# Optimization experiments

Hardware: AMD Instinct MI355X
Metric: run time of the kernel (lower is better)

The kernel has to match this reference:

```python
import jax, jax.numpy as jnp
import numpy as np
from jax.ops import segment_sum

N_NODES = 500_000
N_EDGES = 16_000_000


def gcn_conv(x, W, b, src, dst, n_nodes):
    """PyG GCNConv: linear transform, add self-loops, sym deg norm, scatter-add."""
    xw = x @ W  # [N, out]
    # degree including self-loop (edge weight 1 each)
    deg = segment_sum(jnp.ones((src.shape[0],), xw.dtype), dst, num_segments=n_nodes) + 1.0
    dinv = jax.lax.rsqrt(deg)  # deg^{-1/2}, deg >= 1 so safe
    norm = dinv[src] * dinv[dst]  # [E]
    msg = xw[src] * norm[:, None]  # [E, out]
    agg = segment_sum(msg, dst, num_segments=n_nodes)
    # self-loop contribution: norm_ii = dinv_i^2
    agg = agg + xw * (dinv * dinv)[:, None]
    return agg + b


def setup_inputs() -> dict:
    key = jax.random.key(0)
    ks = jax.random.split(key, 8)
    x = jax.random.normal(ks[0], (N_NODES, 2), dtype=jnp.float32)
    edge_index = jax.random.randint(ks[1], (2, N_EDGES), 0, N_NODES, dtype=jnp.int64)
    def glorot(k, fan_in, fan_out):
        s = jnp.sqrt(6.0 / (fan_in + fan_out))
        return jax.random.uniform(k, (fan_in, fan_out), jnp.float32, -s, s)
    return {
        "x": x,
        "edge_index": edge_index,
        "W1": glorot(ks[2], 2, 4), "b1": jnp.zeros((4,), jnp.float32),
        "W2": glorot(ks[3], 4, 4), "b2": jnp.zeros((4,), jnp.float32),
        "W3": glorot(ks[4], 4, 2), "b3": jnp.zeros((2,), jnp.float32),
    }


def reference(x, edge_index, W1, b1, W2, b2, W3, b3):
    src, dst = edge_index[0], edge_index[1]
    n = x.shape[0]
    h = jnp.tanh(gcn_conv(x, W1, b1, src, dst, n))
    h = jnp.tanh(gcn_conv(h, W2, b2, src, dst, n))
    h = gcn_conv(h, W3, b3, src, dst, n)
    return h
```

## Files before the change

### kernel.cpp

```cpp
#include <hip/hip_runtime.h>
#include <hip/hip_fp16.h>


#define TPB 256
#define T_TILE 16384
#define SBB 12
#define NSB_MAX 128
#define FINE_BITS 10
#define EB_CAP 34048


__global__ void __launch_bounds__(512)
count1(const int* __restrict__ dst, int* __restrict__ cnt1, int ntB, int E, int SB) {
    __shared__ int hist[NSB_MAX];
    int blk = blockIdx.x, tid = threadIdx.x;
    if (tid < SB) hist[tid] = 0;
    __syncthreads();
    int base = blk * T_TILE;
    #pragma unroll 8
    for (int it = 0; it < T_TILE / 512; ++it) {
        int e = base + it * 512 + tid;
        if (e < E) atomicAdd(&hist[((unsigned)dst[e]) >> SBB], 1);
    }
    __syncthreads();
    if (tid < SB) cnt1[(size_t)tid * ntB + blk] = hist[tid];
}

__global__ void scan_k1(const int* __restrict__ data, int* __restrict__ bsum, int len) {
    __shared__ int lds[TPB];
    int b = blockIdx.x, t = threadIdx.x;
    int base = b * 1024 + t * 4;
    int s = 0;
    #pragma unroll
    for (int j = 0; j < 4; ++j) { int i = base + j; if (i < len) s += data[i]; }
    lds[t] = s; __syncthreads();
    for (int off = 128; off > 0; off >>= 1) {
        if (t < off) lds[t] += lds[t + off];
        __syncthreads();
    }
    if (t == 0) bsum[b] = lds[0];
}

__global__ void scan_k2(int* __restrict__ bsum, int NB) {
    __shared__ int lds[1024];
    int t = threadIdx.x;
    int v = (t < NB) ? bsum[t] : 0;
    lds[t] = v; __syncthreads();
    for (int off = 1; off < 1024; off <<= 1) {
        int add = (t >= off) ? lds[t - off] : 0;
        __syncthreads();
        lds[t] += add;
        __syncthreads();
    }
    if (t < NB) bsum[t] = lds[t] - v;
}

__global__ void scan_k3(int* __restrict__ data, const int* __restrict__ bsum, int len) {
    __shared__ int lds[TPB];
    int b = blockIdx.x, t = threadIdx.x;
    int base = b * 1024 + t * 4;
    int v[4]; int s = 0;
    #pragma unroll
    for (int j = 0; j < 4; ++j) { int i = base + j; v[j] = (i < len) ? data[i] : 0; s += v[j]; }
    int orig = s;
    lds[t] = s; __syncthreads();
    for (int off = 1; off < 256; off <<= 1) {
        int add = (t >= off) ? lds[t - off] : 0;
        __syncthreads();
        lds[t] += add;
        __syncthreads();
    }
    int run = bsum[b] + lds[t] - orig;
    #pragma unroll
    for (int j = 0; j < 4; ++j) {
        int i = base + j;
        if (i < len) { data[i] = run; run += v[j]; }
    }
}

__global__ void bases_fix(const int* __restrict__ cnt1, int ntB, int SB,
                          int* __restrict__ bases1, int* __restrict__ rowptr,
                          int N, int E) {
    int t = threadIdx.x;
    if (t < SB) bases1[t] = cnt1[(size_t)t * ntB];
    if (t == 0) { bases1[SB] = E; rowptr[N] = E; }
}

__global__ void __launch_bounds__(512)
scatter1(const int* __restrict__ dst, const int* __restrict__ src,
         const int* __restrict__ cnt1, unsigned* __restrict__ pk1,
         int ntB, int E, int SB) {
    __shared__ unsigned lpk[T_TILE];
    __shared__ int lhist[NSB_MAX];
    __shared__ int lexcl[NSB_MAX];
    __shared__ int lcur[NSB_MAX];
    __shared__ int basec[NSB_MAX];
    int blk = blockIdx.x, tid = threadIdx.x;
    if (tid < NSB_MAX) lhist[tid] = 0;
    if (tid < SB) basec[tid] = cnt1[(size_t)tid * ntB + blk];
    __syncthreads();
    int base = blk * T_TILE;
    #pragma unroll 8
    for (int it = 0; it < T_TILE / 512; ++it) {
        int e = base + it * 512 + tid;
        if (e < E) atomicAdd(&lhist[((unsigned)dst[e]) >> SBB], 1);
    }
    __syncthreads();
    int hv = (tid < NSB_MAX) ? lhist[tid] : 0;
    if (tid < NSB_MAX) lexcl[tid] = hv;
    __syncthreads();
    for (int off = 1; off < NSB_MAX; off <<= 1) {
        int a = (tid < NSB_MAX && tid >= off) ? lexcl[tid - off] : 0;
        __syncthreads();
        if (tid < NSB_MAX) lexcl[tid] += a;
        __syncthreads();
    }
    if (tid < NSB_MAX) { lexcl[tid] -= hv; lcur[tid] = lexcl[tid]; }
    __syncthreads();
    #pragma unroll 8
    for (int it = 0; it < T_TILE / 512; ++it) {
        int e = base + it * 512 + tid;
        if (e < E) {
            unsigned d = (unsigned)dst[e];
            unsigned s = (unsigned)src[e];
            int pos = atomicAdd(&lcur[d >> SBB], 1);
            lpk[pos] = (d & 4095u) | (s << SBB);
        }
    }
    __syncthreads();
    for (int b = 0; b < SB; ++b) {
        int lo = lexcl[b], cntb = lhist[b], gb = basec[b];
        for (int t2 = tid; t2 < cntb; t2 += 512)
            pk1[gb + t2] = lpk[lo + t2];
    }
}

__global__ void __launch_bounds__(1024)
buildfine(const int* __restrict__ bases1, const unsigned* __restrict__ pk1,
          const float* __restrict__ x, int* __restrict__ rowptr,
          float* __restrict__ dinv, unsigned* __restrict__ z1h,
          unsigned* __restrict__ csr, int N) {
    __shared__ int cnt[1024];
    __shared__ int tmp[1024];
    __shared__ int cur[1024];
    __shared__ unsigned eb[EB_CAP];
    __shared__ int redbase;
    int bid = blockIdx.x, tid = threadIdx.x;
    int sb = bid >> 2, j = bid & 3;
    int node0 = (sb << SBB) + (j << FINE_BITS);
    int ebeg = bases1[sb], eend = bases1[sb + 1];
    int n = eend - ebeg;
    cnt[tid] = 0;
    if (tid == 0) redbase = 0;
    __syncthreads();
    int lane = tid & 63;
    int myprev = 0;
    int k0 = 0;
    for (; k0 + 8192 <= n; k0 += 8192) {
        unsigned p[8];
        #pragma unroll
        for (int u = 0; u < 8; ++u) p[u] = pk1[ebeg + k0 + tid + u * 1024];
        #pragma unroll
        for (int u = 0; u < 8; ++u) {
            int f = (int)((p[u] >> FINE_BITS) & 3u);
            myprev += (int)__popcll(__ballot(f < j));
            if (f == j) atomicAdd(&cnt[p[u] & 1023u], 1);
        }
    }
    for (int kk = k0; kk < n; kk += 1024) {
        int k = kk + tid;
        bool valid = (k < n);
        unsigned p = valid ? pk1[ebeg + k] : 0u;
        int f = valid ? (int)((p >> FINE_BITS) & 3u) : 4;
        myprev += (int)__popcll(__ballot(valid && f < j));
        if (valid && f == j) atomicAdd(&cnt[p & 1023u], 1);
    }
    if (lane == 0 && myprev > 0) atomicAdd(&redbase, myprev);
    __syncthreads();
    int csr_base = ebeg + redbase;
    int c = cnt[tid];
    tmp[tid] = c; __syncthreads();
    for (int o = 1; o < 1024; o <<= 1) {
        int a = (tid >= o) ? tmp[tid - o] : 0;
        __syncthreads();
        tmp[tid] += a;
        __syncthreads();
    }
    int excl = tmp[tid] - c;
    int tot = tmp[1023];
    int i = node0 + tid;
    if (i < N) {
        rowptr[i] = csr_base + excl;
        float di = rsqrtf((float)c + 1.0f);
        dinv[i] = di;
        float2 xv = ((const float2*)x)[i];
        __half2 hz = __floats2half2_rn(xv.x * di, xv.y * di);
        z1h[i] = *(unsigned*)&hz;
    }
    cur[tid] = excl;
    __syncthreads();
    if (tot <= EB_CAP) {
        k0 = 0;
        for (; k0 + 8192 <= n; k0 += 8192) {
            unsigned p[8];
            #pragma unroll
            for (int u = 0; u < 8; ++u) p[u] = pk1[ebeg + k0 + tid + u * 1024];
            #pragma unroll
            for (int u = 0; u < 8; ++u) {
                if (((p[u] >> FINE_BITS) & 3u) == (unsigned)j) {
                    int pos = atomicAdd(&cur[p[u] & 1023u], 1);
                    eb[pos] = p[u] >> SBB;
                }
            }
        }
        for (int k = k0 + tid; k < n; k += 1024) {
            unsigned p = pk1[ebeg + k];
            if (((p >> FINE_BITS) & 3u) == (unsigned)j) {
                int pos = atomicAdd(&cur[p & 1023u], 1);
                eb[pos] = p >> SBB;
            }
        }
        __syncthreads();
        for (int k = tid; k < tot; k += 1024) csr[csr_base + k] = eb[k];
    } else {
        for (int k = tid; k < n; k += 1024) {
            unsigned p = pk1[ebeg + k];
            if (((p >> FINE_BITS) & 3u) == (unsigned)j) {
                int pos = atomicAdd(&cur[p & 1023u], 1);
                csr[csr_base + pos] = p >> SBB;
            }
        }
    }
}


__global__ void gcn1(const int* __restrict__ rowptr, const unsigned* __restrict__ csr,
                     const unsigned* __restrict__ z1h, const float* __restrict__ W1,
                     const float* __restrict__ b1, const float* __restrict__ dinv,
                     uint2* __restrict__ z2h, int N) {
    int i = blockIdx.x * blockDim.x + threadIdx.x;
    if (i >= N) return;
    int r0 = rowptr[i], r1 = rowptr[i + 1];
    float a0, a1;
    {
        unsigned zr = z1h[i];
        float2 zi = __half22float2(*(__half2*)&zr);
        a0 = zi.x; a1 = zi.y;
    }
    int k = r0;
    for (; k + 16 <= r1; k += 16) {
        unsigned j[16];
        #pragma unroll
        for (int u = 0; u < 16; ++u) j[u] = __builtin_nontemporal_load(&csr[k + u]);
        unsigned raw[16];
        #pragma unroll
        for (int u = 0; u < 16; ++u) raw[u] = z1h[j[u]];
        #pragma unroll
        for (int u = 0; u < 16; ++u) {
            float2 v = __half22float2(*(__half2*)&raw[u]);
            a0 += v.x; a1 += v.y;
        }
    }
    for (; k < r1; ++k) {
        unsigned zr = z1h[csr[k]];
        float2 zv = __half22float2(*(__half2*)&zr);
        a0 += zv.x; a1 += zv.y;
    }
    float di = dinv[i];
    float g0 = di * a0, g1 = di * a1;
    float o0 = di * tanhf(fmaf(g0, W1[0], fmaf(g1, W1[4], b1[0])));
    float o1 = di * tanhf(fmaf(g0, W1[1], fmaf(g1, W1[5], b1[1])));
    float o2 = di * tanhf(fmaf(g0, W1[2], fmaf(g1, W1[6], b1[2])));
    float o3 = di * tanhf(fmaf(g0, W1[3], fmaf(g1, W1[7], b1[3])));
    __half2 ha = __floats2half2_rn(o0, o1);
    __half2 hb = __floats2half2_rn(o2, o3);
    uint2 packed;
    packed.x = *(unsigned*)&ha;
    packed.y = *(unsigned*)&hb;
    z2h[i] = packed;
}

__global__ void gcn2(const int* __restrict__ rowptr, const unsigned* __restrict__ csr,
                     const uint2* __restrict__ z2h, const float* __restrict__ W2,
                     const float* __restrict__ b2, const float* __restrict__ W3,
                     const float* __restrict__ dinv, unsigned* __restrict__ z3h, int N) {
    int i = blockIdx.x * blockDim.x + threadIdx.x;
    if (i >= N) return;
    int r0 = rowptr[i], r1 = rowptr[i + 1];
    float a0, a1, a2, a3;
    {
        uint2 raw = z2h[i];
        float2 f01 = __half22float2(*(__half2*)&raw.x);
        float2 f23 = __half22float2(*(__half2*)&raw.y);
        a0 = f01.x; a1 = f01.y; a2 = f23.x; a3 = f23.y;
    }
    int k = r0;
    for (; k + 8 <= r1; k += 8) {
        unsigned j[8];
        #pragma unroll
        for (int u = 0; u < 8; ++u) j[u] = __builtin_nontemporal_load(&csr[k + u]);
        uint2 raw[8];
        #pragma unroll
        for (int u = 0; u < 8; ++u) raw[u] = z2h[j[u]];
        #pragma unroll
        for (int u = 0; u < 8; ++u) {
            float2 f01 = __half22float2(*(__half2*)&raw[u].x);
            float2 f23 = __half22float2(*(__half2*)&raw[u].y);
            a0 += f01.x; a1 += f01.y; a2 += f23.x; a3 += f23.y;
        }
    }
    for (; k < r1; ++k) {
        uint2 raw = z2h[csr[k]];
        float2 f01 = __half22float2(*(__half2*)&raw.x);
        float2 f23 = __half22float2(*(__half2*)&raw.y);
        a0 += f01.x; a1 += f01.y; a2 += f23.x; a3 += f23.y;
    }
    float di = dinv[i];
    float g0 = di * a0, g1 = di * a1, g2 = di * a2, g3 = di * a3;
    float h[4];
    #pragma unroll
    for (int c = 0; c < 4; ++c)
        h[c] = tanhf(b2[c] + g0 * W2[c] + g1 * W2[4 + c] + g2 * W2[8 + c] + g3 * W2[12 + c]);
    float v0 = h[0] * W3[0] + h[1] * W3[2] + h[2] * W3[4] + h[3] * W3[6];
    float v1 = h[0] * W3[1] + h[1] * W3[3] + h[2] * W3[5] + h[3] * W3[7];
    __half2 hz = __floats2half2_rn(v0 * di, v1 * di);
    z3h[i] = *(unsigned*)&hz;
}

__global__ void gcn3(const int* __restrict__ rowptr, const unsigned* __restrict__ csr,
                     const unsigned* __restrict__ z3h, const float* __restrict__ b3,
                     const float* __restrict__ dinv, float* __restrict__ out, int N) {
    int i = blockIdx.x * blockDim.x + threadIdx.x;
    if (i >= N) return;
    int r0 = rowptr[i], r1 = rowptr[i + 1];
    float a0, a1;
    {
        unsigned zr = z3h[i];
        float2 zi = __half22float2(*(__half2*)&zr);
        a0 = zi.x; a1 = zi.y;
    }
    int k = r0;
    for (; k + 16 <= r1; k += 16) {
        unsigned j[16];
        #pragma unroll
        for (int u = 0; u < 16; ++u) j[u] = __builtin_nontemporal_load(&csr[k + u]);
        unsigned raw[16];
        #pragma unroll
        for (int u = 0; u < 16; ++u) raw[u] = z3h[j[u]];
        #pragma unroll
        for (int u = 0; u < 16; ++u) {
            float2 v = __half22float2(*(__half2*)&raw[u]);
            a0 += v.x; a1 += v.y;
        }
    }
    for (; k < r1; ++k) {
        unsigned zr = z3h[csr[k]];
        float2 zv = __half22float2(*(__half2*)&zr);
        a0 += zv.x; a1 += zv.y;
    }
    float di = dinv[i];
    ((float2*)out)[i] = make_float2(fmaf(di, a0, b3[0]), fmaf(di, a1, b3[1]));
}

extern "C" void kernel_launch(void* const* d_in, const int* in_sizes, int n_in,
                              void* d_out, int out_size, void* d_ws, size_t ws_size,
                              hipStream_t stream) {
    const float* x  = (const float*)d_in[0];
    const int*   ei = (const int*)d_in[1];
    const float* W1 = (const float*)d_in[2];
    const float* b1 = (const float*)d_in[3];
    const float* W2 = (const float*)d_in[4];
    const float* b2 = (const float*)d_in[5];
    const float* W3 = (const float*)d_in[6];
    const float* b3 = (const float*)d_in[7];
    float* out = (float*)d_out;

    const int N = in_sizes[0] / 2;
    const int E = in_sizes[1] / 2;
    const int* src = ei;
    const int* dst = ei + E;

    const int SB  = (N + (1 << SBB) - 1) >> SBB;
    const int ntB = (E + T_TILE - 1) / T_TILE;
    const int mlen = SB * ntB;
    const int NB = (mlen + 1023) / 1024;

    auto align = [](size_t o) { return (o + 255) & ~(size_t)255; };
    char* wbase = (char*)d_ws;
    size_t off = 0;
    float*    dinv   = (float*)(wbase + off);    off = align(off + (size_t)N * 4);
    unsigned* z1h    = (unsigned*)(wbase + off); off = align(off + (size_t)N * 4);
    uint2*    z2h    = (uint2*)(wbase + off);    off = align(off + (size_t)N * 8);
    unsigned* z3h    = (unsigned*)(wbase + off); off = align(off + (size_t)N * 4);
    int*      rowptr = (int*)(wbase + off);      off = align(off + (size_t)(N + 1) * 4);
    int*      bsum   = (int*)(wbase + off);      off = align(off + (size_t)1024 * 4);
    int*      bases1 = (int*)(wbase + off);      off = align(off + (size_t)(SB + 1) * 4);
    int*      cnt1   = (int*)(wbase + off);      off = align(off + (size_t)mlen * 4);
    unsigned* pk1    = (unsigned*)(wbase + off); off = align(off + (size_t)E * 4);
    unsigned* csr    = (unsigned*)(wbase + off); off = align(off + (size_t)E * 4);

    dim3 gN((N + TPB - 1) / TPB);
    count1<<<dim3(ntB), dim3(512), 0, stream>>>(dst, cnt1, ntB, E, SB);
    scan_k1<<<dim3(NB), dim3(TPB), 0, stream>>>(cnt1, bsum, mlen);
    scan_k2<<<dim3(1), dim3(1024), 0, stream>>>(bsum, NB);
    scan_k3<<<dim3(NB), dim3(TPB), 0, stream>>>(cnt1, bsum, mlen);
    bases_fix<<<dim3(1), dim3(256), 0, stream>>>(cnt1, ntB, SB, bases1, rowptr, N, E);
    scatter1<<<dim3(ntB), dim3(512), 0, stream>>>(dst, src, cnt1, pk1, ntB, E, SB);
    buildfine<<<dim3(SB * 4), dim3(1024), 0, stream>>>(bases1, pk1, x, rowptr, dinv,
                                                       z1h, csr, N);
    gcn1<<<gN, dim3(TPB), 0, stream>>>(rowptr, csr, z1h, W1, b1, dinv, z2h, N);
    gcn2<<<gN, dim3(TPB), 0, stream>>>(rowptr, csr, z2h, W2, b2, W3, dinv, z3h, N);
    gcn3<<<gN, dim3(TPB), 0, stream>>>(rowptr, csr, z3h, b3, dinv, out, N);
}
```

Before: 781.2 us.

## Split layer-2 gather into two passes by source-node half for cache locality

Each CSR row is partitioned so that edges whose source lies in the lower half of the node range come first, and a split pointer is recorded per row. Layer 2 then becomes two kernels: the first gathers only from the lower half of z2h and writes fp32 partial sums, and the second gathers from the upper half, adds the partials and applies the dense transform. Keeping each pass's gather working set to half the feature table (about 2 MB) is meant to improve L2 hit rates on random gathers. The cost is an extra kernel launch, a 16 B-per-node partial-sum round trip, a second row-pointer array, and extra LDS atomics in buildfine.

```diff
diff --git a/kernel.cpp b/kernel.cpp
--- a/kernel.cpp
+++ b/kernel.cpp
@@ -138,11 +138,14 @@
 __global__ void __launch_bounds__(1024)
 buildfine(const int* __restrict__ bases1, const unsigned* __restrict__ pk1,
           const float* __restrict__ x, int* __restrict__ rowptr,
-          float* __restrict__ dinv, unsigned* __restrict__ z1h,
-          unsigned* __restrict__ csr, int N) {
-    __shared__ int cnt[1024];
+          int* __restrict__ splitr, float* __restrict__ dinv,
+          unsigned* __restrict__ z1h, unsigned* __restrict__ csr,
+          int N, unsigned NHP) {
+    __shared__ int cntT[1024];
+    __shared__ int cntA[1024];
     __shared__ int tmp[1024];
-    __shared__ int cur[1024];
+    __shared__ int curA[1024];
+    __shared__ int curB[1024];
     __shared__ unsigned eb[EB_CAP];
     __shared__ int redbase;
     int bid = blockIdx.x, tid = threadIdx.x;
@@ -150,7 +153,7 @@
     int node0 = (sb << SBB) + (j << FINE_BITS);
     int ebeg = bases1[sb], eend = bases1[sb + 1];
     int n = eend - ebeg;
-    cnt[tid] = 0;
+    cntT[tid] = 0; cntA[tid] = 0;
     if (tid == 0) redbase = 0;
     __syncthreads();
     int lane = tid & 63;
@@ -164,7 +167,11 @@
         for (int u = 0; u < 8; ++u) {
             int f = (int)((p[u] >> FINE_BITS) & 3u);
             myprev += (int)__popcll(__ballot(f < j));
-            if (f == j) atomicAdd(&cnt[p[u] & 1023u], 1);
+            if (f == j) {
+                unsigned nd = p[u] & 1023u;
+                atomicAdd(&cntT[nd], 1);
+                if (p[u] < NHP) atomicAdd(&cntA[nd], 1);
+            }
         }
     }
     for (int kk = k0; kk < n; kk += 1024) {
@@ -173,12 +180,17 @@
         unsigned p = valid ? pk1[ebeg + k] : 0u;
         int f = valid ? (int)((p >> FINE_BITS) & 3u) : 4;
         myprev += (int)__popcll(__ballot(valid && f < j));
-        if (valid && f == j) atomicAdd(&cnt[p & 1023u], 1);
+        if (valid && f == j) {
+            unsigned nd = p & 1023u;
+            atomicAdd(&cntT[nd], 1);
+            if (p < NHP) atomicAdd(&cntA[nd], 1);
+        }
     }
     if (lane == 0 && myprev > 0) atomicAdd(&redbase, myprev);
     __syncthreads();
     int csr_base = ebeg + redbase;
-    int c = cnt[tid];
+    int c = cntT[tid];
+    int ca = cntA[tid];
     tmp[tid] = c; __syncthreads();
     for (int o = 1; o < 1024; o <<= 1) {
         int a = (tid >= o) ? tmp[tid - o] : 0;
@@ -191,13 +203,15 @@
     int i = node0 + tid;
     if (i < N) {
         rowptr[i] = csr_base + excl;
+        splitr[i] = csr_base + excl + ca;
         float di = rsqrtf((float)c + 1.0f);
         dinv[i] = di;
         float2 xv = ((const float2*)x)[i];
         __half2 hz = __floats2half2_rn(xv.x * di, xv.y * di);
         z1h[i] = *(unsigned*)&hz;
     }
-    cur[tid] = excl;
+    curA[tid] = excl;
+    curB[tid] = excl + ca;
     __syncthreads();
     if (tot <= EB_CAP) {
         k0 = 0;
@@ -208,7 +222,9 @@
             #pragma unroll
             for (int u = 0; u < 8; ++u) {
                 if (((p[u] >> FINE_BITS) & 3u) == (unsigned)j) {
-                    int pos = atomicAdd(&cur[p[u] & 1023u], 1);
+                    unsigned nd = p[u] & 1023u;
+                    int* cp = (p[u] < NHP) ? curA : curB;
+                    int pos = atomicAdd(&cp[nd], 1);
                     eb[pos] = p[u] >> SBB;
                 }
             }
@@ -216,7 +232,9 @@
         for (int k = k0 + tid; k < n; k += 1024) {
             unsigned p = pk1[ebeg + k];
             if (((p >> FINE_BITS) & 3u) == (unsigned)j) {
-                int pos = atomicAdd(&cur[p & 1023u], 1);
+                unsigned nd = p & 1023u;
+                int* cp = (p < NHP) ? curA : curB;
+                int pos = atomicAdd(&cp[nd], 1);
                 eb[pos] = p >> SBB;
             }
         }
@@ -226,7 +244,9 @@
         for (int k = tid; k < n; k += 1024) {
             unsigned p = pk1[ebeg + k];
             if (((p >> FINE_BITS) & 3u) == (unsigned)j) {
-                int pos = atomicAdd(&cur[p & 1023u], 1);
+                unsigned nd = p & 1023u;
+                int* cp = (p < NHP) ? curA : curB;
+                int pos = atomicAdd(&cp[nd], 1);
                 csr[csr_base + pos] = p >> SBB;
             }
         }
@@ -280,21 +300,73 @@
     z2h[i] = packed;
 }
 
-__global__ void gcn2(const int* __restrict__ rowptr, const unsigned* __restrict__ csr,
-                     const uint2* __restrict__ z2h, const float* __restrict__ W2,
-                     const float* __restrict__ b2, const float* __restrict__ W3,
-                     const float* __restrict__ dinv, unsigned* __restrict__ z3h, int N) {
+__global__ void gcn2a(const int* __restrict__ rowptr, const int* __restrict__ splitr,
+                      const unsigned* __restrict__ csr, const uint2* __restrict__ z2h,
+                      unsigned long long* __restrict__ part, int N, unsigned NH) {
     int i = blockIdx.x * blockDim.x + threadIdx.x;
     if (i >= N) return;
-    int r0 = rowptr[i], r1 = rowptr[i + 1];
-    float a0, a1, a2, a3;
-    {
+    int r0 = rowptr[i], rs = splitr[i];
+    float a0 = 0.f, a1 = 0.f, a2 = 0.f, a3 = 0.f;
+    if ((unsigned)i < NH) {
         uint2 raw = z2h[i];
         float2 f01 = __half22float2(*(__half2*)&raw.x);
         float2 f23 = __half22float2(*(__half2*)&raw.y);
         a0 = f01.x; a1 = f01.y; a2 = f23.x; a3 = f23.y;
     }
     int k = r0;
+    for (; k + 8 <= rs; k += 8) {
+        unsigned j[8];
+        #pragma unroll
+        for (int u = 0; u < 8; ++u) j[u] = __builtin_nontemporal_load(&csr[k + u]);
+        uint2 raw[8];
+        #pragma unroll
+        for (int u = 0; u < 8; ++u) raw[u] = z2h[j[u]];
+        #pragma unroll
+        for (int u = 0; u < 8; ++u) {
+            float2 f01 = __half22float2(*(__half2*)&raw[u].x);
+            float2 f23 = __half22float2(*(__half2*)&raw[u].y);
+            a0 += f01.x; a1 += f01.y; a2 += f23.x; a3 += f23.y;
+        }
+    }
+    for (; k < rs; ++k) {
+        uint2 raw = z2h[csr[k]];
+        float2 f01 = __half22float2(*(__half2*)&raw.x);
+        float2 f23 = __half22float2(*(__half2*)&raw.y);
+        a0 += f01.x; a1 += f01.y; a2 += f23.x; a3 += f23.y;
+    }
+    unsigned long long p0 = (unsigned long long)__float_as_uint(a0) |
+                            ((unsigned long long)__float_as_uint(a1) << 32);
+    unsigned long long p1 = (unsigned long long)__float_as_uint(a2) |
+                            ((unsigned long long)__float_as_uint(a3) << 32);
+    __builtin_nontemporal_store(p0, &part[2 * (size_t)i]);
+    __builtin_nontemporal_store(p1, &part[2 * (size_t)i + 1]);
+}
+
+__global__ void gcn2b(const int* __restrict__ rowptr, const int* __restrict__ splitr,
+                      const unsigned* __restrict__ csr, const uint2* __restrict__ z2h,
+                      const float* __restrict__ W2, const float* __restrict__ b2,
+                      const float* __restrict__ W3, const float* __restrict__ dinv,
+                      const unsigned long long* __restrict__ part,
+                      unsigned* __restrict__ z3h, int N, unsigned NH) {
+    int i = blockIdx.x * blockDim.x + threadIdx.x;
+    if (i >= N) return;
+    int rs = splitr[i], r1 = rowptr[i + 1];
+    float a0, a1, a2, a3;
+    {
+        unsigned long long p0 = __builtin_nontemporal_load(&part[2 * (size_t)i]);
+        unsigned long long p1 = __builtin_nontemporal_load(&part[2 * (size_t)i + 1]);
+        a0 = __uint_as_float((unsigned)p0);
+        a1 = __uint_as_float((unsigned)(p0 >> 32));
+        a2 = __uint_as_float((unsigned)p1);
+        a3 = __uint_as_float((unsigned)(p1 >> 32));
+    }
+    if ((unsigned)i >= NH) {
+        uint2 raw = z2h[i];
+        float2 f01 = __half22float2(*(__half2*)&raw.x);
+        float2 f23 = __half22float2(*(__half2*)&raw.y);
+        a0 += f01.x; a1 += f01.y; a2 += f23.x; a3 += f23.y;
+    }
+    int k = rs;
     for (; k + 8 <= r1; k += 8) {
         unsigned j[8];
         #pragma unroll
@@ -384,6 +456,8 @@
     const int ntB = (E + T_TILE - 1) / T_TILE;
     const int mlen = SB * ntB;
     const int NB = (mlen + 1023) / 1024;
+    const unsigned NH  = (unsigned)(N / 2);
+    const unsigned NHP = NH << SBB;
 
     auto align = [](size_t o) { return (o + 255) & ~(size_t)255; };
     char* wbase = (char*)d_ws;
@@ -392,7 +466,10 @@
     unsigned* z1h    = (unsigned*)(wbase + off); off = align(off + (size_t)N * 4);
     uint2*    z2h    = (uint2*)(wbase + off);    off = align(off + (size_t)N * 8);
     unsigned* z3h    = (unsigned*)(wbase + off); off = align(off + (size_t)N * 4);
+    unsigned long long* part = (unsigned long long*)(wbase + off);
+    off = align(off + (size_t)N * 16);
     int*      rowptr = (int*)(wbase + off);      off = align(off + (size_t)(N + 1) * 4);
+    int*      splitr = (int*)(wbase + off);      off = align(off + (size_t)N * 4);
     int*      bsum   = (int*)(wbase + off);      off = align(off + (size_t)1024 * 4);
     int*      bases1 = (int*)(wbase + off);      off = align(off + (size_t)(SB + 1) * 4);
     int*      cnt1   = (int*)(wbase + off);      off = align(off + (size_t)mlen * 4);
@@ -406,9 +483,11 @@
     scan_k3<<<dim3(NB), dim3(TPB), 0, stream>>>(cnt1, bsum, mlen);
     bases_fix<<<dim3(1), dim3(256), 0, stream>>>(cnt1, ntB, SB, bases1, rowptr, N, E);
     scatter1<<<dim3(ntB), dim3(512), 0, stream>>>(dst, src, cnt1, pk1, ntB, E, SB);
-    buildfine<<<dim3(SB * 4), dim3(1024), 0, stream>>>(bases1, pk1, x, rowptr, dinv,
-                                                       z1h, csr, N);
+    buildfine<<<dim3(SB * 4), dim3(1024), 0, stream>>>(bases1, pk1, x, rowptr, splitr,
+                                                       dinv, z1h, csr, N, NHP);
     gcn1<<<gN, dim3(TPB), 0, stream>>>(rowptr, csr, z1h, W1, b1, dinv, z2h, N);
-    gcn2<<<gN, dim3(TPB), 0, stream>>>(rowptr, csr, z2h, W2, b2, W3, dinv, z3h, N);
+    gcn2a<<<gN, dim3(TPB), 0, stream>>>(rowptr, splitr, csr, z2h, part, N, NH);
+    gcn2b<<<gN, dim3(TPB), 0, stream>>>(rowptr, splitr, csr, z2h, W2, b2, W3, dinv,
+                                        part, z3h, N, NH);
     gcn3<<<gN, dim3(TPB), 0, stream>>>(rowptr, csr, z3h, b3, dinv, out, N);
 }
```

After: 787.5 us. No clear change (+0.8%).

## Replace per-node CSR pull with LDS-accumulated push over source-bucketed edges

Applied to the files above, without the earlier changes.

Drops the full per-node CSR build (fine 4-way split, prefix scans, LDS staging) and instead buckets each destination region's edges by source super-block. Each layer then runs a push kernel where a block gathers source features and accumulates into a 4096-node LDS accumulator with shared-memory float atomics, writing per-quarter partials that a finalize kernel reduces and activates. This aims to make the source gathers more cache-local and to remove the divergent per-row loops, at the cost of LDS atomic contention, partial-buffer traffic and nondeterministic float summation order.

```diff
diff --git a/kernel.cpp b/kernel.cpp
--- a/kernel.cpp
+++ b/kernel.cpp
@@ -6,8 +6,6 @@
 #define T_TILE 16384
 #define SBB 12
 #define NSB_MAX 128
-#define FINE_BITS 10
-#define EB_CAP 34048
 
 
 __global__ void __launch_bounds__(512)
@@ -79,11 +77,10 @@
 }
 
 __global__ void bases_fix(const int* __restrict__ cnt1, int ntB, int SB,
-                          int* __restrict__ bases1, int* __restrict__ rowptr,
-                          int N, int E) {
+                          int* __restrict__ bases1, int E) {
     int t = threadIdx.x;
     if (t < SB) bases1[t] = cnt1[(size_t)t * ntB];
-    if (t == 0) { bases1[SB] = E; rowptr[N] = E; }
+    if (t == 0) bases1[SB] = E;
 }
 
 __global__ void __launch_bounds__(512)
@@ -136,135 +133,172 @@
 }
 
 __global__ void __launch_bounds__(1024)
-buildfine(const int* __restrict__ bases1, const unsigned* __restrict__ pk1,
-          const float* __restrict__ x, int* __restrict__ rowptr,
-          float* __restrict__ dinv, unsigned* __restrict__ z1h,
-          unsigned* __restrict__ csr, int N) {
-    __shared__ int cnt[1024];
-    __shared__ int tmp[1024];
-    __shared__ int cur[1024];
-    __shared__ unsigned eb[EB_CAP];
-    __shared__ int redbase;
-    int bid = blockIdx.x, tid = threadIdx.x;
-    int sb = bid >> 2, j = bid & 3;
-    int node0 = (sb << SBB) + (j << FINE_BITS);
-    int ebeg = bases1[sb], eend = bases1[sb + 1];
+buildpush(const int* __restrict__ bases1, const unsigned* __restrict__ pk1,
+          const float* __restrict__ x, float* __restrict__ dinv,
+          unsigned* __restrict__ z1h, unsigned* __restrict__ pk2,
+          int* __restrict__ tb, int N) {
+    __shared__ int deg[4096];
+    __shared__ int hist[16][NSB_MAX];
+    __shared__ int cnt[NSB_MAX];
+    __shared__ int cur[NSB_MAX];
+    int reg = blockIdx.x, tid = threadIdx.x;
+    int ebeg = bases1[reg], eend = bases1[reg + 1];
     int n = eend - ebeg;
-    cnt[tid] = 0;
-    if (tid == 0) redbase = 0;
-    __syncthreads();
-    int lane = tid & 63;
-    int myprev = 0;
-    int k0 = 0;
-    for (; k0 + 8192 <= n; k0 += 8192) {
-        unsigned p[8];
-        #pragma unroll
-        for (int u = 0; u < 8; ++u) p[u] = pk1[ebeg + k0 + tid + u * 1024];
-        #pragma unroll
-        for (int u = 0; u < 8; ++u) {
-            int f = (int)((p[u] >> FINE_BITS) & 3u);
-            myprev += (int)__popcll(__ballot(f < j));
-            if (f == j) atomicAdd(&cnt[p[u] & 1023u], 1);
+    int w = tid >> 6;
+    for (int i = tid; i < 4096; i += 1024) deg[i] = 0;
+    for (int i = tid; i < 16 * NSB_MAX; i += 1024) ((int*)hist)[i] = 0;
+    __syncthreads();
+    for (int k = tid; k < n; k += 1024) {
+        unsigned p = pk1[ebeg + k];
+        atomicAdd(&deg[p & 4095u], 1);
+        atomicAdd(&hist[w][p >> 24], 1);
+    }
+    __syncthreads();
+    if (tid < NSB_MAX) {
+        int s = 0;
+        #pragma unroll
+        for (int r = 0; r < 16; ++r) s += hist[r][tid];
+        cnt[tid] = s;
+        cur[tid] = s;
+    }
+    __syncthreads();
+    for (int off = 1; off < NSB_MAX; off <<= 1) {
+        int a = (tid < NSB_MAX && tid >= off) ? cur[tid - off] : 0;
+        __syncthreads();
+        if (tid < NSB_MAX) cur[tid] += a;
+        __syncthreads();
+    }
+    if (tid < NSB_MAX) {
+        int excl = cur[tid] - cnt[tid];
+        tb[reg * 129 + tid] = ebeg + excl;
+        cur[tid] = excl;
+    }
+    if (tid == 0) tb[reg * 129 + 128] = eend;
+    int node0 = reg << SBB;
+    for (int t = tid; t < 4096; t += 1024) {
+        int i = node0 + t;
+        if (i < N) {
+            float di = rsqrtf((float)deg[t] + 1.0f);
+            dinv[i] = di;
+            float2 xv = ((const float2*)x)[i];
+            __half2 hz = __floats2half2_rn(xv.x * di, xv.y * di);
+            z1h[i] = *(unsigned*)&hz;
         }
     }
-    for (int kk = k0; kk < n; kk += 1024) {
-        int k = kk + tid;
-        bool valid = (k < n);
-        unsigned p = valid ? pk1[ebeg + k] : 0u;
-        int f = valid ? (int)((p >> FINE_BITS) & 3u) : 4;
-        myprev += (int)__popcll(__ballot(valid && f < j));
-        if (valid && f == j) atomicAdd(&cnt[p & 1023u], 1);
-    }
-    if (lane == 0 && myprev > 0) atomicAdd(&redbase, myprev);
-    __syncthreads();
-    int csr_base = ebeg + redbase;
-    int c = cnt[tid];
-    tmp[tid] = c; __syncthreads();
-    for (int o = 1; o < 1024; o <<= 1) {
-        int a = (tid >= o) ? tmp[tid - o] : 0;
-        __syncthreads();
-        tmp[tid] += a;
-        __syncthreads();
-    }
-    int excl = tmp[tid] - c;
-    int tot = tmp[1023];
-    int i = node0 + tid;
-    if (i < N) {
-        rowptr[i] = csr_base + excl;
-        float di = rsqrtf((float)c + 1.0f);
-        dinv[i] = di;
-        float2 xv = ((const float2*)x)[i];
-        __half2 hz = __floats2half2_rn(xv.x * di, xv.y * di);
-        z1h[i] = *(unsigned*)&hz;
-    }
-    cur[tid] = excl;
-    __syncthreads();
-    if (tot <= EB_CAP) {
-        k0 = 0;
-        for (; k0 + 8192 <= n; k0 += 8192) {
-            unsigned p[8];
-            #pragma unroll
-            for (int u = 0; u < 8; ++u) p[u] = pk1[ebeg + k0 + tid + u * 1024];
-            #pragma unroll
-            for (int u = 0; u < 8; ++u) {
-                if (((p[u] >> FINE_BITS) & 3u) == (unsigned)j) {
-                    int pos = atomicAdd(&cur[p[u] & 1023u], 1);
-                    eb[pos] = p[u] >> SBB;
-                }
-            }
+    __syncthreads();
+    for (int k = tid; k < n; k += 1024) {
+        unsigned p = pk1[ebeg + k];
+        int pos = atomicAdd(&cur[p >> 24], 1);
+        pk2[ebeg + pos] = p;
+    }
+}
+
+
+__global__ void __launch_bounds__(512)
+push_f2(const unsigned* __restrict__ pk2, const int* __restrict__ tb,
+        const unsigned* __restrict__ zt, float* __restrict__ partial) {
+    __shared__ float acc[8192];
+    int bx = blockIdx.x, tid = threadIdx.x;
+    int reg = bx >> 2, s = bx & 3;
+    for (int i = tid; i < 8192; i += 512) acc[i] = 0.f;
+    __syncthreads();
+    int e0 = tb[reg * 129 + 32 * s];
+    int e1 = tb[reg * 129 + 32 * (s + 1)];
+    int k = e0;
+    for (; k + 2048 <= e1; k += 2048) {
+        unsigned p[4];
+        #pragma unroll
+        for (int u = 0; u < 4; ++u) p[u] = __builtin_nontemporal_load(&pk2[k + tid + u * 512]);
+        unsigned zr[4];
+        #pragma unroll
+        for (int u = 0; u < 4; ++u) zr[u] = zt[p[u] >> SBB];
+        #pragma unroll
+        for (int u = 0; u < 4; ++u) {
+            float2 v = __half22float2(*(__half2*)&zr[u]);
+            unsigned d = (p[u] & 4095u) << 1;
+            atomicAdd(&acc[d], v.x);
+            atomicAdd(&acc[d + 1], v.y);
         }
-        for (int k = k0 + tid; k < n; k += 1024) {
-            unsigned p = pk1[ebeg + k];
-            if (((p >> FINE_BITS) & 3u) == (unsigned)j) {
-                int pos = atomicAdd(&cur[p & 1023u], 1);
-                eb[pos] = p >> SBB;
-            }
+    }
+    for (int kk = k + tid; kk < e1; kk += 512) {
+        unsigned p = pk2[kk];
+        unsigned zr = zt[p >> SBB];
+        float2 v = __half22float2(*(__half2*)&zr);
+        unsigned d = (p & 4095u) << 1;
+        atomicAdd(&acc[d], v.x);
+        atomicAdd(&acc[d + 1], v.y);
+    }
+    __syncthreads();
+    float* pout = partial + (size_t)bx * 8192;
+    for (int i = tid; i < 8192; i += 512) pout[i] = acc[i];
+}
+
+__global__ void __launch_bounds__(512)
+push_f4(const unsigned* __restrict__ pk2, const int* __restrict__ tb,
+        const unsigned long long* __restrict__ zt, float* __restrict__ partial) {
+    __shared__ float acc[16384];
+    int bx = blockIdx.x, tid = threadIdx.x;
+    int reg = bx >> 2, s = bx & 3;
+    for (int i = tid; i < 16384; i += 512) acc[i] = 0.f;
+    __syncthreads();
+    int e0 = tb[reg * 129 + 32 * s];
+    int e1 = tb[reg * 129 + 32 * (s + 1)];
+    int k = e0;
+    for (; k + 2048 <= e1; k += 2048) {
+        unsigned p[4];
+        #pragma unroll
+        for (int u = 0; u < 4; ++u) p[u] = __builtin_nontemporal_load(&pk2[k + tid + u * 512]);
+        unsigned long long zr[4];
+        #pragma unroll
+        for (int u = 0; u < 4; ++u) zr[u] = zt[p[u] >> SBB];
+        #pragma unroll
+        for (int u = 0; u < 4; ++u) {
+            unsigned lo = (unsigned)zr[u], hi = (unsigned)(zr[u] >> 32);
+            float2 f01 = __half22float2(*(__half2*)&lo);
+            float2 f23 = __half22float2(*(__half2*)&hi);
+            unsigned d = (p[u] & 4095u) << 2;
+            atomicAdd(&acc[d], f01.x);
+            atomicAdd(&acc[d + 1], f01.y);
+            atomicAdd(&acc[d + 2], f23.x);
+            atomicAdd(&acc[d + 3], f23.y);
         }
-        __syncthreads();
-        for (int k = tid; k < tot; k += 1024) csr[csr_base + k] = eb[k];
-    } else {
-        for (int k = tid; k < n; k += 1024) {
-            unsigned p = pk1[ebeg + k];
-            if (((p >> FINE_BITS) & 3u) == (unsigned)j) {
-                int pos = atomicAdd(&cur[p & 1023u], 1);
-                csr[csr_base + pos] = p >> SBB;
-            }
-        }
-    }
-}
-
-
-__global__ void gcn1(const int* __restrict__ rowptr, const unsigned* __restrict__ csr,
-                     const unsigned* __restrict__ z1h, const float* __restrict__ W1,
-                     const float* __restrict__ b1, const float* __restrict__ dinv,
-                     uint2* __restrict__ z2h, int N) {
+    }
+    for (int kk = k + tid; kk < e1; kk += 512) {
+        unsigned p = pk2[kk];
+        unsigned long long zr = zt[p >> SBB];
+        unsigned lo = (unsigned)zr, hi = (unsigned)(zr >> 32);
+        float2 f01 = __half22float2(*(__half2*)&lo);
+        float2 f23 = __half22float2(*(__half2*)&hi);
+        unsigned d = (p & 4095u) << 2;
+        atomicAdd(&acc[d], f01.x);
+        atomicAdd(&acc[d + 1], f01.y);
+        atomicAdd(&acc[d + 2], f23.x);
+        atomicAdd(&acc[d + 3], f23.y);
+    }
+    __syncthreads();
+    float* pout = partial + (size_t)bx * 16384;
+    for (int i = tid; i < 16384; i += 512) pout[i] = acc[i];
+}
+
+
+__global__ void fin1(const float* __restrict__ partial, const unsigned* __restrict__ z1h,
+                     const float* __restrict__ dinv, const float* __restrict__ W1,
+                     const float* __restrict__ b1, unsigned long long* __restrict__ z2h,
+                     int N) {
     int i = blockIdx.x * blockDim.x + threadIdx.x;
     if (i >= N) return;
-    int r0 = rowptr[i], r1 = rowptr[i + 1];
+    int reg = i >> SBB, t = i & 4095;
     float a0, a1;
     {
         unsigned zr = z1h[i];
-        float2 zi = __half22float2(*(__half2*)&zr);
-        a0 = zi.x; a1 = zi.y;
-    }
-    int k = r0;
-    for (; k + 16 <= r1; k += 16) {
-        unsigned j[16];
-        #pragma unroll
-        for (int u = 0; u < 16; ++u) j[u] = __builtin_nontemporal_load(&csr[k + u]);
-        unsigned raw[16];
-        #pragma unroll
-        for (int u = 0; u < 16; ++u) raw[u] = z1h[j[u]];
-        #pragma unroll
-        for (int u = 0; u < 16; ++u) {
-            float2 v = __half22float2(*(__half2*)&raw[u]);
-            a0 += v.x; a1 += v.y;
-        }
-    }
-    for (; k < r1; ++k) {
-        unsigned zr = z1h[csr[k]];
-        float2 zv = __half22float2(*(__half2*)&zr);
-        a0 += zv.x; a1 += zv.y;
+        float2 z = __half22float2(*(__half2*)&zr);
+        a0 = z.x; a1 = z.y;
+    }
+    #pragma unroll
+    for (int s = 0; s < 4; ++s) {
+        size_t b = ((size_t)(reg * 4 + s) * 4096 + t) * 2;
+        a0 += partial[b];
+        a1 += partial[b + 1];
     }
     float di = dinv[i];
     float g0 = di * a0, g1 = di * a1;
@@ -274,46 +308,34 @@
     float o3 = di * tanhf(fmaf(g0, W1[3], fmaf(g1, W1[7], b1[3])));
     __half2 ha = __floats2half2_rn(o0, o1);
     __half2 hb = __floats2half2_rn(o2, o3);
-    uint2 packed;
-    packed.x = *(unsigned*)&ha;
-    packed.y = *(unsigned*)&hb;
-    z2h[i] = packed;
-}
-
-__global__ void gcn2(const int* __restrict__ rowptr, const unsigned* __restrict__ csr,
-                     const uint2* __restrict__ z2h, const float* __restrict__ W2,
+    unsigned long long pk = (unsigned long long)(*(unsigned*)&ha) |
+                            ((unsigned long long)(*(unsigned*)&hb) << 32);
+    z2h[i] = pk;
+}
+
+__global__ void fin2(const float* __restrict__ partial,
+                     const unsigned long long* __restrict__ z2h,
+                     const float* __restrict__ dinv, const float* __restrict__ W2,
                      const float* __restrict__ b2, const float* __restrict__ W3,
-                     const float* __restrict__ dinv, unsigned* __restrict__ z3h, int N) {
+                     unsigned* __restrict__ z3h, int N) {
     int i = blockIdx.x * blockDim.x + threadIdx.x;
     if (i >= N) return;
-    int r0 = rowptr[i], r1 = rowptr[i + 1];
+    int reg = i >> SBB, t = i & 4095;
     float a0, a1, a2, a3;
     {
-        uint2 raw = z2h[i];
-        float2 f01 = __half22float2(*(__half2*)&raw.x);
-        float2 f23 = __half22float2(*(__half2*)&raw.y);
+        unsigned long long zr = z2h[i];
+        unsigned lo = (unsigned)zr, hi = (unsigned)(zr >> 32);
+        float2 f01 = __half22float2(*(__half2*)&lo);
+        float2 f23 = __half22float2(*(__half2*)&hi);
         a0 = f01.x; a1 = f01.y; a2 = f23.x; a3 = f23.y;
     }
-    int k = r0;
-    for (; k + 8 <= r1; k += 8) {
-        unsigned j[8];
-        #pragma unroll
-        for (int u = 0; u < 8; ++u) j[u] = __builtin_nontemporal_load(&csr[k + u]);
-        uint2 raw[8];
-        #pragma unroll
-        for (int u = 0; u < 8; ++u) raw[u] = z2h[j[u]];
-        #pragma unroll
-        for (int u = 0; u < 8; ++u) {
-            float2 f01 = __half22float2(*(__half2*)&raw[u].x);
-            float2 f23 = __half22float2(*(__half2*)&raw[u].y);
-            a0 += f01.x; a1 += f01.y; a2 += f23.x; a3 += f23.y;
-        }
-    }
-    for (; k < r1; ++k) {
-        uint2 raw = z2h[csr[k]];
-        float2 f01 = __half22float2(*(__half2*)&raw.x);
-        float2 f23 = __half22float2(*(__half2*)&raw.y);
-        a0 += f01.x; a1 += f01.y; a2 += f23.x; a3 += f23.y;
+    #pragma unroll
+    for (int s = 0; s < 4; ++s) {
+        size_t b = ((size_t)(reg * 4 + s) * 4096 + t) * 4;
+        a0 += partial[b];
+        a1 += partial[b + 1];
+        a2 += partial[b + 2];
+        a3 += partial[b + 3];
     }
     float di = dinv[i];
     float g0 = di * a0, g1 = di * a1, g2 = di * a2, g3 = di * a3;
@@ -327,36 +349,23 @@
     z3h[i] = *(unsigned*)&hz;
 }
 
-__global__ void gcn3(const int* __restrict__ rowptr, const unsigned* __restrict__ csr,
-                     const unsigned* __restrict__ z3h, const float* __restrict__ b3,
-                     const float* __restrict__ dinv, float* __restrict__ out, int N) {
+__global__ void fin3(const float* __restrict__ partial, const unsigned* __restrict__ z3h,
+                     const float* __restrict__ dinv, const float* __restrict__ b3,
+                     float* __restrict__ out, int N) {
     int i = blockIdx.x * blockDim.x + threadIdx.x;
     if (i >= N) return;
-    int r0 = rowptr[i], r1 = rowptr[i + 1];
+    int reg = i >> SBB, t = i & 4095;
     float a0, a1;
     {
         unsigned zr = z3h[i];
-        float2 zi = __half22float2(*(__half2*)&zr);
-        a0 = zi.x; a1 = zi.y;
-    }
-    int k = r0;
-    for (; k + 16 <= r1; k += 16) {
-        unsigned j[16];
-        #pragma unroll
-        for (int u = 0; u < 16; ++u) j[u] = __builtin_nontemporal_load(&csr[k + u]);
-        unsigned raw[16];
-        #pragma unroll
-        for (int u = 0; u < 16; ++u) raw[u] = z3h[j[u]];
-        #pragma unroll
-        for (int u = 0; u < 16; ++u) {
-            float2 v = __half22float2(*(__half2*)&raw[u]);
-            a0 += v.x; a1 += v.y;
-        }
-    }
-    for (; k < r1; ++k) {
-        unsigned zr = z3h[csr[k]];
-        float2 zv = __half22float2(*(__half2*)&zr);
-        a0 += zv.x; a1 += zv.y;
+        float2 z = __half22float2(*(__half2*)&zr);
+        a0 = z.x; a1 = z.y;
+    }
+    #pragma unroll
+    for (int s = 0; s < 4; ++s) {
+        size_t b = ((size_t)(reg * 4 + s) * 4096 + t) * 2;
+        a0 += partial[b];
+        a1 += partial[b + 1];
     }
     float di = dinv[i];
     ((float2*)out)[i] = make_float2(fmaf(di, a0, b3[0]), fmaf(di, a1, b3[1]));
@@ -390,25 +399,30 @@
     size_t off = 0;
     float*    dinv   = (float*)(wbase + off);    off = align(off + (size_t)N * 4);
     unsigned* z1h    = (unsigned*)(wbase + off); off = align(off + (size_t)N * 4);
-    uint2*    z2h    = (uint2*)(wbase + off);    off = align(off + (size_t)N * 8);
+    unsigned long long* z2h = (unsigned long long*)(wbase + off);
+    off = align(off + (size_t)N * 8);
     unsigned* z3h    = (unsigned*)(wbase + off); off = align(off + (size_t)N * 4);
-    int*      rowptr = (int*)(wbase + off);      off = align(off + (size_t)(N + 1) * 4);
+    int*      tb     = (int*)(wbase + off);      off = align(off + (size_t)SB * 129 * 4);
     int*      bsum   = (int*)(wbase + off);      off = align(off + (size_t)1024 * 4);
     int*      bases1 = (int*)(wbase + off);      off = align(off + (size_t)(SB + 1) * 4);
     int*      cnt1   = (int*)(wbase + off);      off = align(off + (size_t)mlen * 4);
     unsigned* pk1    = (unsigned*)(wbase + off); off = align(off + (size_t)E * 4);
-    unsigned* csr    = (unsigned*)(wbase + off); off = align(off + (size_t)E * 4);
+    unsigned* pk2    = (unsigned*)(wbase + off); off = align(off + (size_t)E * 4);
+    float* partial = (float*)pk1;
 
     dim3 gN((N + TPB - 1) / TPB);
     count1<<<dim3(ntB), dim3(512), 0, stream>>>(dst, cnt1, ntB, E, SB);
     scan_k1<<<dim3(NB), dim3(TPB), 0, stream>>>(cnt1, bsum, mlen);
     scan_k2<<<dim3(1), dim3(1024), 0, stream>>>(bsum, NB);
     scan_k3<<<dim3(NB), dim3(TPB), 0, stream>>>(cnt1, bsum, mlen);
-    bases_fix<<<dim3(1), dim3(256), 0, stream>>>(cnt1, ntB, SB, bases1, rowptr, N, E);
+    bases_fix<<<dim3(1), dim3(256), 0, stream>>>(cnt1, ntB, SB, bases1, E);
     scatter1<<<dim3(ntB), dim3(512), 0, stream>>>(dst, src, cnt1, pk1, ntB, E, SB);
-    buildfine<<<dim3(SB * 4), dim3(1024), 0, stream>>>(bases1, pk1, x, rowptr, dinv,
-                                                       z1h, csr, N);
-    gcn1<<<gN, dim3(TPB), 0, stream>>>(rowptr, csr, z1h, W1, b1, dinv, z2h, N);
-    gcn2<<<gN, dim3(TPB), 0, stream>>>(rowptr, csr, z2h, W2, b2, W3, dinv, z3h, N);
-    gcn3<<<gN, dim3(TPB), 0, stream>>>(rowptr, csr, z3h, b3, dinv, out, N);
-}
+    buildpush<<<dim3(SB), dim3(1024), 0, stream>>>(bases1, pk1, x, dinv, z1h, pk2, tb, N);
+
+    push_f2<<<dim3(SB * 4), dim3(512), 0, stream>>>(pk2, tb, z1h, partial);
+    fin1<<<gN, dim3(TPB), 0, stream>>>(partial, z1h, dinv, W1, b1, z2h, N);
+    push_f4<<<dim3(SB * 4), dim3(512), 0, stream>>>(pk2, tb, z2h, partial);
+    fin2<<<gN, dim3(TPB), 0, stream>>>(partial, z2h, dinv, W2, b2, W3, z3h, N);
+    push_f2<<<dim3(SB * 4), dim3(512), 0, stream>>>(pk2, tb, z3h, partial);
+    fin3<<<gN, dim3(TPB), 0, stream>>>(partial, z3h, dinv, b3, out, N);
+}
```

Result: slower. 1.192 ms (+52.6%).
